# Kernel tuning notes

Measured on AMD Instinct MI355X. Metric: run time of the kernel, lower is better.

The kernel has to match this reference:

```python
import jax, jax.numpy as jnp
import numpy as np

B, QL, KL = 2, 1024, 4096
H = 1024          # hidden_size
NH = 16           # num_heads
HD = H // NH      # head_dim = 64


def setup_inputs() -> dict:
    key = jax.random.key(0)
    k1, k2, k3, k4, k5 = jax.random.split(key, 5)
    s = 1.0 / np.sqrt(H)
    return {
        "query": jax.random.normal(k1, (B, QL, H), dtype=jnp.float32),
        "key_value": jax.random.normal(k2, (B, KL, H), dtype=jnp.float32),
        "w_q": jax.random.uniform(k3, (H, H), dtype=jnp.float32, minval=-s, maxval=s),
        "w_kv": jax.random.uniform(k4, (H, 2 * H), dtype=jnp.float32, minval=-s, maxval=s),
        "w_out": jax.random.uniform(k5, (H, H), dtype=jnp.float32, minval=-s, maxval=s),
    }


def reference(query, key_value, w_q, w_kv, w_out):
    # projections
    q = (query @ w_q).reshape(B, QL, NH, HD).transpose(0, 2, 1, 3)      # [B,NH,QL,HD]
    kv = (key_value @ w_kv).reshape(B, KL, 2, NH, HD)
    k = kv[:, :, 0].transpose(0, 2, 1, 3)                               # [B,NH,KL,HD]
    v = kv[:, :, 1].transpose(0, 2, 1, 3)                               # [B,NH,KL,HD]
    # scaled dot-product attention (explicit, matching source)
    scale = 1.0 / np.sqrt(HD).astype(np.float32)
    attn = jnp.einsum("bhqd,bhkd->bhqk", q, k) * scale                  # [B,NH,QL,KL]
    attn = jax.nn.softmax(attn, axis=-1)
    out = jnp.einsum("bhqk,bhkd->bhqd", attn, v)                        # [B,NH,QL,HD]
    out = out.transpose(0, 2, 1, 3).reshape(B, QL, H)
    return out @ w_out
```

## Files before the change

kernel.cpp:

```cpp
#include <hip/hip_runtime.h>

#define Bb   2
#define QL   1024
#define KL   4096
#define Hh   1024
#define NH   16
#define HD   64

#define KSPLIT 2
#define CHUNK  (KL / KSPLIT)
#define NTT    (CHUNK / 64)

typedef unsigned short u16;
typedef __attribute__((ext_vector_type(8))) short bf16x8;
typedef __attribute__((ext_vector_type(8))) unsigned short usv8;
typedef __attribute__((ext_vector_type(4))) float f32x4;

#define QSCALE 0.1803368801111204f
#define RTHR   11.0f

__device__ __forceinline__ u16 f2bf(float f) {
    union { float f; unsigned int u; } v; v.f = f;
    unsigned int r = (v.u + 0x7FFFu + ((v.u >> 16) & 1u)) >> 16;
    return (u16)r;
}

__device__ __forceinline__ unsigned int cvt_pk_bf16(float lo, float hi) {
    unsigned int r;
    asm("v_cvt_pk_bf16_f32 %0, %1, %2" : "=v"(r) : "v"(lo), "v"(hi));
    return r;
}

__device__ __forceinline__ float max3f(float a, float b, float c) {
    float r;
    asm("v_max3_f32 %0, %1, %2, %3" : "=v"(r) : "v"(a), "v"(b), "v"(c));
    return r;
}

__device__ __forceinline__ void gload16(const void* g, void* l) {
    __builtin_amdgcn_global_load_lds(
        (const __attribute__((address_space(1))) void*)g,
        (__attribute__((address_space(3))) void*)l, 16, 0, 0);
}

__device__ __forceinline__ uint4 pack8(const float4& f0, const float4& f1) {
    uint4 o;
    o.x = cvt_pk_bf16(f0.x, f0.y);
    o.y = cvt_pk_bf16(f0.z, f0.w);
    o.z = cvt_pk_bf16(f1.x, f1.y);
    o.w = cvt_pk_bf16(f1.z, f1.w);
    return o;
}

__global__ __launch_bounds__(256) void wtrans_all(const float* __restrict__ wq,
                                                  const float* __restrict__ wkv,
                                                  const float* __restrict__ wout,
                                                  u16* __restrict__ wqT,
                                                  u16* __restrict__ wkvT,
                                                  u16* __restrict__ woutT) {
    __shared__ float T[64][65];
    int bid = blockIdx.x;
    const float* in; u16* out; int C;
    if (bid < 256)      { in = wq;   out = wqT;   C = 1024; }
    else if (bid < 768) { in = wkv;  out = wkvT;  C = 2048; bid -= 256; }
    else                { in = wout; out = woutT; C = 1024; bid -= 768; }
    const int nc = C >> 6;
    const int c0 = (bid % nc) * 64;
    const int r0 = (bid / nc) * 64;
    const int t  = threadIdx.x;
    const int tx = t & 15, ty = t >> 4;
#pragma unroll
    for (int p = 0; p < 4; ++p) {
        const int r = ty + p * 16;
        float4 v = *reinterpret_cast<const float4*>(in + (size_t)(r0 + r) * C + c0 + tx * 4);
        T[r][tx * 4 + 0] = v.x; T[r][tx * 4 + 1] = v.y;
        T[r][tx * 4 + 2] = v.z; T[r][tx * 4 + 3] = v.w;
    }
    __syncthreads();
#pragma unroll
    for (int p = 0; p < 4; ++p) {
        const int c = ty + p * 16;
        const int n = c0 + c;
        ushort4 o;
        o.x = f2bf(T[tx * 4 + 0][c]); o.y = f2bf(T[tx * 4 + 1][c]);
        o.z = f2bf(T[tx * 4 + 2][c]); o.w = f2bf(T[tx * 4 + 3][c]);
        const int kb   = r0 + tx * 4;
        const int kout = (kb & ~63) | ((((kb >> 3) & 7) ^ (n & 7)) << 3) | (kb & 7);
        *reinterpret_cast<ushort4*>(out + (size_t)n * 1024 + kout) = o;
    }
}

__global__ __launch_bounds__(256) void qkvgemm(const float* __restrict__ Aq32,
                                               const float* __restrict__ Akv32,
                                               const u16* __restrict__ wqT,
                                               const u16* __restrict__ wkvT,
                                               u16* __restrict__ Qb,
                                               u16* __restrict__ KT,
                                               u16* __restrict__ VT) {
    __shared__ u16 As[128 * 64];
    __shared__ u16 Bs[128 * 64];
    const int tid = threadIdx.x, lane = tid & 63, w = tid >> 6;
    const int wr = w >> 1, wc = w & 1;
    const int x7 = lane & 7;
    const int lrow = lane >> 3, lcol = (lane & 7) * 8;
    const int arow = tid >> 3, acol8 = (tid & 7) * 8;
    const int aphys = acol8 ^ ((arow & 7) << 3);

    if (blockIdx.x < 1024) {
        const int id = blockIdx.x;
        const int sw = (id & 7) * 128 + (id >> 3);
        const int bx = sw % 16, by = sw / 16;
        const int row0 = by * 128, col0 = bx * 128;
        const int MROW = wr * 64;

        f32x4 acc[4][4];
#pragma unroll
        for (int m = 0; m < 4; ++m)
#pragma unroll
            for (int n = 0; n < 4; ++n) acc[m][n] = (f32x4){0.f, 0.f, 0.f, 0.f};

        auto stage = [&](int k0) {
            __syncthreads();
#pragma unroll
            for (int p = 0; p < 4; ++p) {
                const int r = p * 32 + arow;
                const float* src = Akv32 + (size_t)(row0 + r) * 1024 + k0 + acol8;
                float4 f0 = *reinterpret_cast<const float4*>(src);
                float4 f1 = *reinterpret_cast<const float4*>(src + 4);
                *reinterpret_cast<uint4*>(&As[r * 64 + aphys]) = pack8(f0, f1);
            }
#pragma unroll
            for (int p = 0; p < 4; ++p) {
                const int base = w * 512 + p * 2048;
                const int row  = (base >> 6) + lrow;
                gload16(wkvT + (size_t)(col0 + row) * 1024 + k0 + lcol, &Bs[base]);
            }
            __syncthreads();
        };

        if (col0 < 1024) {
            for (int k0 = 0; k0 < 1024; k0 += 64) {
                stage(k0);
#pragma unroll
                for (int kk = 0; kk < 2; ++kk) {
                    bf16x8 af[4], bfr[4];
                    const int G = ((kk * 4 + (lane >> 4)) ^ x7) * 8;
#pragma unroll
                    for (int m = 0; m < 4; ++m)
                        af[m] = *reinterpret_cast<const bf16x8*>(
                            &As[(MROW + m * 16 + (lane & 15)) * 64 + G]);
#pragma unroll
                    for (int n = 0; n < 4; ++n)
                        bfr[n] = *reinterpret_cast<const bf16x8*>(
                            &Bs[(wc * 64 + n * 16 + (lane & 15)) * 64 + G]);
#pragma unroll
                    for (int m = 0; m < 4; ++m)
#pragma unroll
                        for (int n = 0; n < 4; ++n)
                            acc[m][n] = __builtin_amdgcn_mfma_f32_16x16x32_bf16(
                                bfr[n], af[m], acc[m][n], 0, 0, 0);
                }
            }
#pragma unroll
            for (int m = 0; m < 4; ++m) {
                const int gr  = row0 + MROW + m * 16 + (lane & 15);
                const int b   = gr >> 12;
                const int k   = gr & 4095;
                const int kt_i = k >> 6, k_in = k & 63;
#pragma unroll
                for (int n = 0; n < 4; ++n) {
                    const int gc0 = col0 + wc * 64 + n * 16 + (lane >> 4) * 4;
                    const int h   = gc0 >> 6, d0 = gc0 & 63;
                    u16* blob = KT + (((size_t)((b << 4) + h) * 64 + kt_i) << 9) * 8;
                    const int og = k_in * 8 + ((d0 >> 3) ^ (k_in & 7));
                    ushort4 pk;
                    pk.x = f2bf(acc[m][n][0]); pk.y = f2bf(acc[m][n][1]);
                    pk.z = f2bf(acc[m][n][2]); pk.w = f2bf(acc[m][n][3]);
                    *reinterpret_cast<ushort4*>(&blob[og * 8 + (d0 & 7)]) = pk;
                }
            }
        } else {
            for (int k0 = 0; k0 < 1024; k0 += 64) {
                stage(k0);
#pragma unroll
                for (int kk = 0; kk < 2; ++kk) {
                    bf16x8 af[4], bfr[4];
                    const int G = ((kk * 4 + (lane >> 4)) ^ x7) * 8;
#pragma unroll
                    for (int m = 0; m < 4; ++m)
                        af[m] = *reinterpret_cast<const bf16x8*>(
                            &As[(MROW + m * 16 + (lane & 15)) * 64 + G]);
#pragma unroll
                    for (int n = 0; n < 4; ++n)
                        bfr[n] = *reinterpret_cast<const bf16x8*>(
                            &Bs[(wc * 64 + n * 16 + (lane & 15)) * 64 + G]);
#pragma unroll
                    for (int m = 0; m < 4; ++m)
#pragma unroll
                        for (int n = 0; n < 4; ++n)
                            acc[m][n] = __builtin_amdgcn_mfma_f32_16x16x32_bf16(
                                af[m], bfr[n], acc[m][n], 0, 0, 0);
                }
            }
#pragma unroll
            for (int m = 0; m < 4; ++m) {
                const int gr0 = row0 + MROW + m * 16 + (lane >> 4) * 4;
                const int b   = gr0 >> 12;
                const int k   = gr0 & 4095;
                const int kt_i = k >> 6, k_in = k & 63;
#pragma unroll
                for (int n = 0; n < 4; ++n) {
                    const int gc = col0 + wc * 64 + n * 16 + (lane & 15);
                    const int h  = (gc & 1023) >> 6, d = gc & 63;
                    u16* blob = VT + (((size_t)((b << 4) + h) * 64 + kt_i) << 9) * 8;
                    const int og = d * 8 + ((k_in >> 3) ^ (d & 7));
                    ushort4 pk;
                    pk.x = f2bf(acc[m][n][0]); pk.y = f2bf(acc[m][n][1]);
                    pk.z = f2bf(acc[m][n][2]); pk.w = f2bf(acc[m][n][3]);
                    *reinterpret_cast<ushort4*>(&blob[og * 8 + (k_in & 7)]) = pk;
                }
            }
        }
    } else {
        const int id = blockIdx.x - 1024;
        const int sw = (id & 7) * 32 + (id >> 3);
        const int bx = sw % 8, by = sw / 8;
        const int row0 = by * 64, col0 = bx * 128;
        const int MROW = wr * 32;

        f32x4 acc[2][4];
#pragma unroll
        for (int m = 0; m < 2; ++m)
#pragma unroll
            for (int n = 0; n < 4; ++n) acc[m][n] = (f32x4){0.f, 0.f, 0.f, 0.f};

        for (int k0 = 0; k0 < 1024; k0 += 64) {
            __syncthreads();
#pragma unroll
            for (int p = 0; p < 2; ++p) {
                const int r = p * 32 + arow;
                const float* src = Aq32 + (size_t)(row0 + r) * 1024 + k0 + acol8;
                float4 f0 = *reinterpret_cast<const float4*>(src);
                float4 f1 = *reinterpret_cast<const float4*>(src + 4);
                *reinterpret_cast<uint4*>(&As[r * 64 + aphys]) = pack8(f0, f1);
            }
#pragma unroll
            for (int p = 0; p < 4; ++p) {
                const int base = w * 512 + p * 2048;
                const int row  = (base >> 6) + lrow;
                gload16(wqT + (size_t)(col0 + row) * 1024 + k0 + lcol, &Bs[base]);
            }
            __syncthreads();
#pragma unroll
            for (int kk = 0; kk < 2; ++kk) {
                bf16x8 af[2], bfr[4];
                const int G = ((kk * 4 + (lane >> 4)) ^ x7) * 8;
#pragma unroll
                for (int m = 0; m < 2; ++m)
                    af[m] = *reinterpret_cast<const bf16x8*>(
                        &As[(MROW + m * 16 + (lane & 15)) * 64 + G]);
#pragma unroll
                for (int n = 0; n < 4; ++n)
                    bfr[n] = *reinterpret_cast<const bf16x8*>(
                        &Bs[(wc * 64 + n * 16 + (lane & 15)) * 64 + G]);
#pragma unroll
                for (int m = 0; m < 2; ++m)
#pragma unroll
                    for (int n = 0; n < 4; ++n)
                        acc[m][n] = __builtin_amdgcn_mfma_f32_16x16x32_bf16(
                            af[m], bfr[n], acc[m][n], 0, 0, 0);
            }
        }
#pragma unroll
        for (int m = 0; m < 2; ++m)
#pragma unroll
            for (int n = 0; n < 4; ++n) {
                const int gc = col0 + wc * 64 + n * 16 + (lane & 15);
#pragma unroll
                for (int r = 0; r < 4; ++r) {
                    const int gr = row0 + MROW + m * 16 + (lane >> 4) * 4 + r;
                    Qb[(size_t)gr * 1024 + gc] = f2bf(acc[m][n][r] * QSCALE);
                }
            }
    }
}

__global__ __launch_bounds__(256, 2) void attn_mfma(const u16* __restrict__ Qb,
                                                    const u16* __restrict__ KT,
                                                    const u16* __restrict__ VT2,
                                                    float* __restrict__ Op,
                                                    float* __restrict__ m_ws,
                                                    float* __restrict__ l_ws) {
    __shared__ u16 Ks[2][4096];
    __shared__ u16 Vs[2][4096];
    __shared__ u16 Ps[4][2][1024];

    const int bid0 = blockIdx.x;
    const int bid  = (bid0 & 7) * 64 + (bid0 >> 3);
    const int qb   = bid & 7;
    const int h    = (bid >> 3) & 15;
    const int b    = (bid >> 7) & 1;
    const int c    = bid >> 8;
    const int tid  = threadIdx.x;
    const int lane = tid & 63;
    const int w    = tid >> 6;
    const int q_l  = lane & 15;
    const int g    = lane >> 4;
    const int qs7  = q_l & 7;
    const int q0   = qb * 128;
    const int bh   = b * NH + h;

    bf16x8 qa[2][2];
#pragma unroll
    for (int qh = 0; qh < 2; ++qh) {
        const u16* qsrc = Qb + (size_t)(b * QL + q0 + w * 32 + qh * 16 + q_l) * Hh
                          + h * HD + g * 8;
        qa[qh][0] = *reinterpret_cast<const bf16x8*>(qsrc);
        qa[qh][1] = *reinterpret_cast<const bf16x8*>(qsrc + 32);
    }
    asm volatile("s_waitcnt vmcnt(0)" ::: "memory");

    bf16x8 ones;
#pragma unroll
    for (int e = 0; e < 8; ++e) ones[e] = (short)0x3F80;

    float m_i[2] = {-1e30f, -1e30f};
    f32x4 acc_l[2] = {(f32x4){0.f, 0.f, 0.f, 0.f}, (f32x4){0.f, 0.f, 0.f, 0.f}};
    f32x4 acc_o[2][4];
#pragma unroll
    for (int qh = 0; qh < 2; ++qh)
#pragma unroll
        for (int n = 0; n < 4; ++n) acc_o[qh][n] = (f32x4){0.f, 0.f, 0.f, 0.f};

    const int koffA = (g ^ qs7) * 8;
    const int koffB = ((g + 4) ^ qs7) * 8;
    const int rowq  = q_l * 64;
    const u16* KsA[2] = { &Ks[0][rowq + koffA], &Ks[1][rowq + koffA] };
    const u16* KsB[2] = { &Ks[0][rowq + koffB], &Ks[1][rowq + koffB] };
    const u16* VsA[2] = { &Vs[0][rowq + koffA], &Vs[1][rowq + koffA] };
    const u16* VsB[2] = { &Vs[0][rowq + koffB], &Vs[1][rowq + koffB] };
    const u16* PsRA = &Ps[w][0][rowq + koffA];
    const u16* PsRB = &Ps[w][0][rowq + koffB];
    u16* PsW[4];
#pragma unroll
    for (int n = 0; n < 4; ++n)
        PsW[n] = &Ps[w][0][rowq + (((2 * n + (g >> 1)) ^ qs7) << 3) + (g & 1) * 4];

    const size_t tb0 = ((size_t)bh * 64 + c * NTT) * 4096;
    const u16* kpt = KT  + tb0 + (size_t)(w * 64 + lane) * 8 + 1024;
    const u16* vpt = VT2 + tb0 + (size_t)(w * 64 + lane) * 8 + 1024;
    u16* kdst[2] = { &Ks[0][w * 512], &Ks[1][w * 512] };
    u16* vdst[2] = { &Vs[0][w * 512], &Vs[1][w * 512] };

    gload16(kpt - 1024, kdst[0]);
    gload16(kpt + 1024, kdst[0] + 2048);
    gload16(vpt - 1024, vdst[0]);
    gload16(vpt + 1024, vdst[0] + 2048);

    auto tile = [&](int CUR, int t) {
        __builtin_amdgcn_s_barrier();
        if (t + 1 < NTT) {
            kpt += 4096; vpt += 4096;
            gload16(kpt - 1024, kdst[CUR ^ 1]);
            gload16(kpt + 1024, kdst[CUR ^ 1] + 2048);
            gload16(vpt - 1024, vdst[CUR ^ 1]);
            gload16(vpt + 1024, vdst[CUR ^ 1] + 2048);
            asm volatile("s_waitcnt vmcnt(4)" ::: "memory");
        } else {
            asm volatile("s_waitcnt vmcnt(0)" ::: "memory");
        }
        __builtin_amdgcn_sched_barrier(0);
        __builtin_amdgcn_s_barrier();

        f32x4 s[2][4];
        __builtin_amdgcn_s_setprio(1);
#pragma unroll
        for (int n = 0; n < 4; ++n) {
            bf16x8 a0 = *reinterpret_cast<const bf16x8*>(KsA[CUR] + n * 1024);
            bf16x8 a1 = *reinterpret_cast<const bf16x8*>(KsB[CUR] + n * 1024);
#pragma unroll
            for (int qh = 0; qh < 2; ++qh) {
                f32x4 z = (f32x4){0.f, 0.f, 0.f, 0.f};
                z = __builtin_amdgcn_mfma_f32_16x16x32_bf16(a0, qa[qh][0], z, 0, 0, 0);
                z = __builtin_amdgcn_mfma_f32_16x16x32_bf16(a1, qa[qh][1], z, 0, 0, 0);
                s[qh][n] = z;
            }
        }
        __builtin_amdgcn_s_setprio(0);

        float mloc[2];
#pragma unroll
        for (int qh = 0; qh < 2; ++qh) {
            float c1 = max3f(s[qh][0][0], s[qh][0][1], s[qh][0][2]);
            c1 = max3f(c1, s[qh][0][3], s[qh][1][0]);
            c1 = max3f(c1, s[qh][1][1], s[qh][1][2]);
            c1 = fmaxf(c1, s[qh][1][3]);
            float c2 = max3f(s[qh][2][0], s[qh][2][1], s[qh][2][2]);
            c2 = max3f(c2, s[qh][2][3], s[qh][3][0]);
            c2 = max3f(c2, s[qh][3][1], s[qh][3][2]);
            c2 = fmaxf(c2, s[qh][3][3]);
            float m = fmaxf(c1, c2);
            m = fmaxf(m, __shfl_xor(m, 16));
            m = fmaxf(m, __shfl_xor(m, 32));
            mloc[qh] = m;
        }
        if (__any((mloc[0] > m_i[0] + RTHR) || (mloc[1] > m_i[1] + RTHR))) {
#pragma unroll
            for (int qh = 0; qh < 2; ++qh) {
                const float mnew = fmaxf(m_i[qh], mloc[qh]);
                const float al   = exp2f(m_i[qh] - mnew);
                m_i[qh] = mnew;
                acc_l[qh][0] *= al; acc_l[qh][1] *= al;
                acc_l[qh][2] *= al; acc_l[qh][3] *= al;
#pragma unroll
                for (int n = 0; n < 4; ++n) {
                    f32x4 tt = acc_o[qh][n];
                    tt[0] *= al; tt[1] *= al; tt[2] *= al; tt[3] *= al;
                    acc_o[qh][n] = tt;
                }
            }
        }
#pragma unroll
        for (int qh = 0; qh < 2; ++qh) {
#pragma unroll
            for (int n = 0; n < 4; ++n)
#pragma unroll
                for (int r = 0; r < 4; ++r) s[qh][n][r] = exp2f(s[qh][n][r] - m_i[qh]);
#pragma unroll
            for (int n = 0; n < 4; ++n) {
                uint2 pk2;
                pk2.x = cvt_pk_bf16(s[qh][n][0], s[qh][n][1]);
                pk2.y = cvt_pk_bf16(s[qh][n][2], s[qh][n][3]);
                *reinterpret_cast<uint2*>(PsW[n] + qh * 1024) = pk2;
            }
        }
        asm volatile("s_waitcnt lgkmcnt(0)" ::: "memory");
        __builtin_amdgcn_sched_barrier(0);

        __builtin_amdgcn_s_setprio(1);
#pragma unroll
        for (int kf = 0; kf < 2; ++kf) {
            const u16* pr = (kf == 0) ? PsRA : PsRB;
            bf16x8 pf0 = *reinterpret_cast<const bf16x8*>(pr);
            bf16x8 pf1 = *reinterpret_cast<const bf16x8*>(pr + 1024);
            acc_l[0] = __builtin_amdgcn_mfma_f32_16x16x32_bf16(ones, pf0, acc_l[0], 0, 0, 0);
            acc_l[1] = __builtin_amdgcn_mfma_f32_16x16x32_bf16(ones, pf1, acc_l[1], 0, 0, 0);
#pragma unroll
            for (int n = 0; n < 4; ++n) {
                const u16* vb = (kf == 0) ? VsA[CUR] : VsB[CUR];
                bf16x8 vf = *reinterpret_cast<const bf16x8*>(vb + n * 1024);
                acc_o[0][n] = __builtin_amdgcn_mfma_f32_16x16x32_bf16(vf, pf0, acc_o[0][n], 0, 0, 0);
                acc_o[1][n] = __builtin_amdgcn_mfma_f32_16x16x32_bf16(vf, pf1, acc_o[1][n], 0, 0, 0);
            }
        }
        __builtin_amdgcn_s_setprio(0);
    };

    for (int t = 0; t < NTT; t += 2) {
        tile(0, t);
        tile(1, t + 1);
    }

#pragma unroll
    for (int qh = 0; qh < 2; ++qh) {
        float* opc = Op + (size_t)c * ((size_t)Bb * QL * Hh)
                     + (size_t)(b * QL + q0 + w * 32 + qh * 16 + q_l) * Hh + h * HD;
#pragma unroll
        for (int n = 0; n < 4; ++n) {
            float4 v = make_float4(acc_o[qh][n][0], acc_o[qh][n][1],
                                   acc_o[qh][n][2], acc_o[qh][n][3]);
            *reinterpret_cast<float4*>(opc + n * 16 + g * 4) = v;
        }
        if (g == 0) {
            const int idx = ((c * Bb + b) * NH + h) * QL + q0 + w * 32 + qh * 16 + q_l;
            m_ws[idx] = m_i[qh];
            l_ws[idx] = acc_l[qh][0];
        }
    }
}

__global__ __launch_bounds__(256) void ogemm(const float* __restrict__ Op,
                                             const float* __restrict__ m_ws,
                                             const float* __restrict__ l_ws,
                                             const u16* __restrict__ Bt,
                                             float* __restrict__ C) {
    __shared__ u16 As[64 * 64];
    __shared__ u16 Bs[128 * 64];
    const int nwg = gridDim.x * gridDim.y;
    const int id  = blockIdx.y * gridDim.x + blockIdx.x;
    const int sw  = (id & 7) * (nwg >> 3) + (id >> 3);
    const int bx  = sw % gridDim.x, by = sw / gridDim.x;
    const int tid = threadIdx.x, lane = tid & 63, w = tid >> 6;
    const int wr = w >> 1, wc = w & 1;
    const int row0 = by * 64, col0 = bx * 128;
    const int MROW = wr * 32;
    const int x7   = lane & 7;

    f32x4 acc[2][4];
#pragma unroll
    for (int m = 0; m < 2; ++m)
#pragma unroll
        for (int n = 0; n < 4; ++n) acc[m][n] = (f32x4){0.f, 0.f, 0.f, 0.f};

    const int lrow = lane >> 3, lcol = (lane & 7) * 8;
    const int arow = tid >> 3, acol8 = (tid & 7) * 8;
    const int aphys = acol8 ^ ((arow & 7) << 3);

    for (int k0 = 0; k0 < 1024; k0 += 64) {
        __syncthreads();
        const int h_ = k0 >> 6;
#pragma unroll
        for (int p = 0; p < 2; ++p) {
            const int r    = p * 32 + arow;
            const int grow = row0 + r;
            const int b_   = grow >> 10, q_ = grow & 1023;
            const int idx  = (((b_ << 4) + h_) << 10) + q_;
            const float m0 = m_ws[idx], m1 = m_ws[idx + 32768];
            const float l0 = l_ws[idx], l1 = l_ws[idx + 32768];
            const float ms = fmaxf(m0, m1);
            float a0 = exp2f(m0 - ms), a1 = exp2f(m1 - ms);
            const float inv = 1.f / (l0 * a0 + l1 * a1);
            a0 *= inv; a1 *= inv;
            const float* o0 = Op + (size_t)grow * 1024 + k0 + acol8;
            const float* o1 = o0 + (size_t)Bb * QL * Hh;
            float4 x0 = *reinterpret_cast<const float4*>(o0);
            float4 x1 = *reinterpret_cast<const float4*>(o0 + 4);
            float4 y0 = *reinterpret_cast<const float4*>(o1);
            float4 y1 = *reinterpret_cast<const float4*>(o1 + 4);
            float4 f0 = make_float4(x0.x * a0 + y0.x * a1, x0.y * a0 + y0.y * a1,
                                    x0.z * a0 + y0.z * a1, x0.w * a0 + y0.w * a1);
            float4 f1 = make_float4(x1.x * a0 + y1.x * a1, x1.y * a0 + y1.y * a1,
                                    x1.z * a0 + y1.z * a1, x1.w * a0 + y1.w * a1);
            *reinterpret_cast<uint4*>(&As[r * 64 + aphys]) = pack8(f0, f1);
        }
#pragma unroll
        for (int p = 0; p < 4; ++p) {
            const int base = w * 512 + p * 2048;
            const int row  = (base >> 6) + lrow;
            gload16(Bt + (size_t)(col0 + row) * 1024 + k0 + lcol, &Bs[base]);
        }
        __syncthreads();
#pragma unroll
        for (int kk = 0; kk < 2; ++kk) {
            bf16x8 af[2], bfr[4];
            const int G = ((kk * 4 + (lane >> 4)) ^ x7) * 8;
#pragma unroll
            for (int m = 0; m < 2; ++m)
                af[m] = *reinterpret_cast<const bf16x8*>(
                    &As[(MROW + m * 16 + (lane & 15)) * 64 + G]);
#pragma unroll
            for (int n = 0; n < 4; ++n)
                bfr[n] = *reinterpret_cast<const bf16x8*>(
                    &Bs[(wc * 64 + n * 16 + (lane & 15)) * 64 + G]);
#pragma unroll
            for (int m = 0; m < 2; ++m)
#pragma unroll
                for (int n = 0; n < 4; ++n)
                    acc[m][n] = __builtin_amdgcn_mfma_f32_16x16x32_bf16(
                        af[m], bfr[n], acc[m][n], 0, 0, 0);
        }
    }
#pragma unroll
    for (int m = 0; m < 2; ++m)
#pragma unroll
        for (int n = 0; n < 4; ++n) {
            const int gc = col0 + wc * 64 + n * 16 + (lane & 15);
#pragma unroll
            for (int r = 0; r < 4; ++r) {
                const int gr = row0 + MROW + m * 16 + (lane >> 4) * 4 + r;
                C[(size_t)gr * 1024 + gc] = acc[m][n][r];
            }
        }
}

extern "C" void kernel_launch(void* const* d_in, const int* in_sizes, int n_in,
                              void* d_out, int out_size, void* d_ws, size_t ws_size,
                              hipStream_t stream) {
    const float* query     = (const float*)d_in[0];
    const float* key_value = (const float*)d_in[1];
    const float* w_q       = (const float*)d_in[2];
    const float* w_kv      = (const float*)d_in[3];
    const float* w_out     = (const float*)d_in[4];
    float* out = (float*)d_out;

    char* ws = (char*)d_ws;
    const size_t MB = 1024 * 1024;
    u16*   KT    = (u16*)(ws);
    u16*   VT    = (u16*)(ws + 16 * MB);
    float* Opart = (float*)(ws + 32 * MB);
    u16*   Qb    = (u16*)(ws + 48 * MB);
    u16*   wkvT  = (u16*)(ws + 52 * MB);
    u16*   wqT   = (u16*)(ws + 56 * MB);
    u16*   woutT = (u16*)(ws + 58 * MB);
    float* m_wsp = (float*)(ws + 60 * MB);
    float* l_wsp = (float*)(ws + 60 * MB + 256 * 1024);

    dim3 blk(256);

    wtrans_all<<<1024, blk, 0, stream>>>(w_q, w_kv, w_out, wqT, wkvT, woutT);

    qkvgemm<<<1280, blk, 0, stream>>>(query, key_value, wqT, wkvT, Qb, KT, VT);

    attn_mfma<<<dim3(KSPLIT * 256), blk, 0, stream>>>(
        Qb, KT, VT, Opart, m_wsp, l_wsp);

    ogemm<<<dim3(8, 32), blk, 0, stream>>>(Opart, m_wsp, l_wsp, woutT, out);
}
```

Measured before the change: 181.6 us.

## Pre-cast activations to bf16 and stage GEMM A tiles via direct global-to-LDS loads

Adds a separate cast kernel that converts the query and key_value activations to bf16 in workspace. The QKV GEMM then loads its A tiles with swizzled global_load_lds, like the B tiles, instead of loading fp32 through registers and converting inside the GEMM loop. This removes the per-block conversion work and the register staging, and lets each tile be converted once instead of once per column block that reads it. In exchange it adds a kernel launch and an extra bf16 write and read pass through workspace memory. kvbf aliases the Opart region, which is only written later by attn_mfma.

```diff
diff --git a/kernel.cpp b/kernel.cpp
--- a/kernel.cpp
+++ b/kernel.cpp
@@ -50,6 +50,20 @@
     o.z = cvt_pk_bf16(f1.x, f1.y);
     o.w = cvt_pk_bf16(f1.z, f1.w);
     return o;
+}
+
+__global__ __launch_bounds__(256) void cast_all(const float* __restrict__ q,
+                                                const float* __restrict__ kv,
+                                                u16* __restrict__ qb,
+                                                u16* __restrict__ kvb) {
+    int bid = blockIdx.x;
+    const float* in; u16* out;
+    if (bid < 1024) { in = q;  out = qb;  }
+    else            { in = kv; out = kvb; bid -= 1024; }
+    const size_t i = ((size_t)bid * 256 + threadIdx.x) * 8;
+    float4 f0 = *reinterpret_cast<const float4*>(in + i);
+    float4 f1 = *reinterpret_cast<const float4*>(in + i + 4);
+    *reinterpret_cast<uint4*>(out + i) = pack8(f0, f1);
 }
 
 __global__ __launch_bounds__(256) void wtrans_all(const float* __restrict__ wq,
@@ -90,8 +104,8 @@
     }
 }
 
-__global__ __launch_bounds__(256) void qkvgemm(const float* __restrict__ Aq32,
-                                               const float* __restrict__ Akv32,
+__global__ __launch_bounds__(256) void qkvgemm(const u16* __restrict__ Aq,
+                                               const u16* __restrict__ Akv,
                                                const u16* __restrict__ wqT,
                                                const u16* __restrict__ wkvT,
                                                u16* __restrict__ Qb,
@@ -103,8 +117,7 @@
     const int wr = w >> 1, wc = w & 1;
     const int x7 = lane & 7;
     const int lrow = lane >> 3, lcol = (lane & 7) * 8;
-    const int arow = tid >> 3, acol8 = (tid & 7) * 8;
-    const int aphys = acol8 ^ ((arow & 7) << 3);
+    const int swcol = lcol ^ ((lrow & 7) << 3);
 
     if (blockIdx.x < 1024) {
         const int id = blockIdx.x;
@@ -123,16 +136,9 @@
             __syncthreads();
 #pragma unroll
             for (int p = 0; p < 4; ++p) {
-                const int r = p * 32 + arow;
-                const float* src = Akv32 + (size_t)(row0 + r) * 1024 + k0 + acol8;
-                float4 f0 = *reinterpret_cast<const float4*>(src);
-                float4 f1 = *reinterpret_cast<const float4*>(src + 4);
-                *reinterpret_cast<uint4*>(&As[r * 64 + aphys]) = pack8(f0, f1);
-            }
-#pragma unroll
-            for (int p = 0; p < 4; ++p) {
                 const int base = w * 512 + p * 2048;
                 const int row  = (base >> 6) + lrow;
+                gload16(Akv + (size_t)(row0 + row) * 1024 + k0 + swcol, &As[base]);
                 gload16(wkvT + (size_t)(col0 + row) * 1024 + k0 + lcol, &Bs[base]);
             }
             __syncthreads();
@@ -238,11 +244,9 @@
             __syncthreads();
 #pragma unroll
             for (int p = 0; p < 2; ++p) {
-                const int r = p * 32 + arow;
-                const float* src = Aq32 + (size_t)(row0 + r) * 1024 + k0 + acol8;
-                float4 f0 = *reinterpret_cast<const float4*>(src);
-                float4 f1 = *reinterpret_cast<const float4*>(src + 4);
-                *reinterpret_cast<uint4*>(&As[r * 64 + aphys]) = pack8(f0, f1);
+                const int base = w * 512 + p * 2048;
+                const int row  = (base >> 6) + lrow;
+                gload16(Aq + (size_t)(row0 + row) * 1024 + k0 + swcol, &As[base]);
             }
 #pragma unroll
             for (int p = 0; p < 4; ++p) {
@@ -587,6 +591,7 @@
     const size_t MB = 1024 * 1024;
     u16*   KT    = (u16*)(ws);
     u16*   VT    = (u16*)(ws + 16 * MB);
+    u16*   kvbf  = (u16*)(ws + 32 * MB);
     float* Opart = (float*)(ws + 32 * MB);
     u16*   Qb    = (u16*)(ws + 48 * MB);
     u16*   wkvT  = (u16*)(ws + 52 * MB);
@@ -594,12 +599,14 @@
     u16*   woutT = (u16*)(ws + 58 * MB);
     float* m_wsp = (float*)(ws + 60 * MB);
     float* l_wsp = (float*)(ws + 60 * MB + 256 * 1024);
+    u16*   qbf   = (u16*)(ws + 64 * MB);
 
     dim3 blk(256);
 
     wtrans_all<<<1024, blk, 0, stream>>>(w_q, w_kv, w_out, wqT, wkvT, woutT);
-
-    qkvgemm<<<1280, blk, 0, stream>>>(query, key_value, wqT, wkvT, Qb, KT, VT);
+    cast_all<<<5120, blk, 0, stream>>>(query, key_value, qbf, kvbf);
+
+    qkvgemm<<<1280, blk, 0, stream>>>(qbf, kvbf, wqT, wkvT, Qb, KT, VT);
 
     attn_mfma<<<dim3(KSPLIT * 256), blk, 0, stream>>>(
         Qb, KT, VT, Opart, m_wsp, l_wsp);
```

New measurement: 174.5 us. 3.9% less time.
